# Optimization experiments

Measured on AMD Instinct MI355X. Metric: run time of the kernel, lower is better.

Reference implementation:

```python
import jax, jax.numpy as jnp
import numpy as np

B, L, D, H, DK, DV = 2, 2048, 512, 8, 64, 64
EPS_LN = 1e-6


def setup_inputs() -> dict:
    key = jax.random.key(0)
    ks = jax.random.split(key, 14)
    ws = 0.02  # weight init scale
    inp = {}
    for i, n in enumerate(["q_r", "q_i", "k_r", "k_i", "v_r", "v_i"]):
        inp[n] = jax.random.normal(ks[i], (B, L, D), jnp.float32)
    for j, n in enumerate(["wq_r", "wq_i", "wk_r", "wk_i", "wv_r", "wv_i", "fc_r", "fc_i"]):
        inp[n] = jax.random.normal(ks[6 + j], (D, D), jnp.float32) * ws
    # complextorch CVLayerNorm affine: (2,2,D) weight, diag = 1/sqrt(2); complex bias = 0
    c = np.float32(1.0 / np.sqrt(2.0))
    ln_w = jnp.zeros((2, 2, D), jnp.float32).at[0, 0].set(c).at[1, 1].set(c)
    inp["ln_w"] = ln_w
    inp["ln_b_r"] = jnp.zeros((D,), jnp.float32)
    inp["ln_b_i"] = jnp.zeros((D,), jnp.float32)
    return inp


def _cv_layernorm(x, ln_w, ln_b_r, ln_b_i):
    # covariance-whitening complex LayerNorm over last dim (complextorch style)
    xr, xi = jnp.real(x), jnp.imag(x)
    xr = xr - jnp.mean(xr, axis=-1, keepdims=True)
    xi = xi - jnp.mean(xi, axis=-1, keepdims=True)
    vrr = jnp.mean(xr * xr, axis=-1, keepdims=True) + EPS_LN
    vii = jnp.mean(xi * xi, axis=-1, keepdims=True) + EPS_LN
    vri = jnp.mean(xr * xi, axis=-1, keepdims=True)
    s = jnp.sqrt(vrr * vii - vri * vri)
    t = jnp.sqrt(vrr + vii + 2.0 * s)
    inv = 1.0 / (s * t)
    rrr, rii, rri = (vii + s) * inv, (vrr + s) * inv, -vri * inv
    yr = rrr * xr + rri * xi
    yi = rri * xr + rii * xi
    out_r = ln_w[0, 0] * yr + ln_w[0, 1] * yi + ln_b_r
    out_i = ln_w[1, 0] * yr + ln_w[1, 1] * yi + ln_b_i
    return out_r, out_i


def _mha(q_r, q_i, k_r, k_i, v_r, v_i, wq_r, wq_i, wk_r, wk_i, wv_r, wv_i,
         fc_r, fc_i, ln_w, ln_b_r, ln_b_i):
    q = (q_r + 1j * q_i).astype(jnp.complex64)
    k = (k_r + 1j * k_i).astype(jnp.complex64)
    v = (v_r + 1j * v_i).astype(jnp.complex64)
    Wq = (wq_r + 1j * wq_i).astype(jnp.complex64)
    Wk = (wk_r + 1j * wk_i).astype(jnp.complex64)
    Wv = (wv_r + 1j * wv_i).astype(jnp.complex64)
    Wfc = (fc_r + 1j * fc_i).astype(jnp.complex64)
    b, lq = q.shape[0], q.shape[1]
    # complex linear projections (torch Linear: y = x @ W^T), split into heads
    qh = jnp.einsum('bld,ed->ble', q, Wq).reshape(b, lq, H, DK).transpose(0, 2, 1, 3)
    kh = jnp.einsum('bld,ed->ble', k, Wk).reshape(b, -1, H, DK).transpose(0, 2, 1, 3)
    vh = jnp.einsum('bld,ed->ble', v, Wv).reshape(b, -1, H, DV).transpose(0, 2, 1, 3)
    temp = jnp.float32(DK ** 0.5)
    attn = jnp.einsum('bhqd,bhkd->bhqk', qh / temp, kh)  # [B,H,Lq,Lk] complex
    # CVSoftMax: softmax over magnitude, phase preserved
    mag = jnp.abs(attn)
    w = jax.nn.softmax(mag, axis=-1)
    attn = (w * jnp.exp(1j * jnp.angle(attn))).astype(jnp.complex64)
    out = jnp.einsum('bhqk,bhkd->bhqd', attn, vh)
    out = out.transpose(0, 2, 1, 3).reshape(b, lq, H * DV)
    out = jnp.einsum('ble,de->bld', out, Wfc)
    x = out + q  # residual (dropout is identity at p=0 / eval)
    return _cv_layernorm(x, ln_w, ln_b_r, ln_b_i)


def reference(q_r, q_i, k_r, k_i, v_r, v_i, wq_r, wq_i, wk_r, wk_i, wv_r, wv_i,
              fc_r, fc_i, ln_w, ln_b_r, ln_b_i):
    out_r, out_i = _mha(q_r, q_i, k_r, k_i, v_r, v_i, wq_r, wq_i, wk_r, wk_i,
                        wv_r, wv_i, fc_r, fc_i, ln_w, ln_b_r, ln_b_i)
    # stack real/imag so output is a real float32 tensor [B, L, D, 2]
    return jnp.stack([out_r, out_i], axis=-1)
```

## Files before the change

### kernel.cpp

```cpp
#include <hip/hip_runtime.h>
#include <hip/hip_bf16.h>
#include <math.h>

#define NB 2
#define NL 2048
#define ND 512
#define NH 8
#define NDK 64
#define NROW (NB*NL)
#define HEADSZ (NB*NH*NL*NDK)
#define SEG_BIG ((size_t)NROW*ND)

typedef __attribute__((ext_vector_type(8))) short bf16x8;
typedef __attribute__((ext_vector_type(4))) float f32x4;

__device__ __align__(16) short g_bq_r[HEADSZ], g_bq_i[HEADSZ];
__device__ __align__(16) short g_bk_r[HEADSZ], g_bk_i[HEADSZ];
__device__ __align__(16) short g_bv_r[HEADSZ], g_bv_i[HEADSZ];
__device__ __align__(16) short g_bo_r[SEG_BIG], g_bo_i[SEG_BIG];
__device__ float g_x_r[SEG_BIG];
__device__ float g_x_i[SEG_BIG];

static __device__ __forceinline__ unsigned pack_bf2(float lo, float hi) {
    __hip_bfloat162 h = __float22bfloat162_rn(make_float2(lo, hi));
    unsigned u;
    __builtin_memcpy(&u, &h, 4);
    return u;
}
static __device__ __forceinline__ uint4 ld_cvt(const float* p) {
    const float4 a = *(const float4*)p;
    const float4 b = *(const float4*)(p + 4);
    uint4 o;
    o.x = pack_bf2(a.x, a.y); o.y = pack_bf2(a.z, a.w);
    o.z = pack_bf2(b.x, b.y); o.w = pack_bf2(b.z, b.w);
    return o;
}
static __device__ __forceinline__ bf16x8 negbf(bf16x8 v) {
    #pragma unroll
    for (int e = 0; e < 8; ++e) v[e] ^= (short)0x8000;
    return v;
}

struct GPtrs {
    const float* xr[3]; const float* xi[3];
    const float* wr[4]; const float* wi[4];
    const float* rr; const float* ri;
};

template<int MODE>
__global__ __launch_bounds__(256, 2)
void bgemm(GPtrs gp)
{
    __shared__ __align__(16) short sAr[64][64], sAi[64][64];
    __shared__ __align__(16) short sBr[64][64], sBi[64][64];

    const int bm = blockIdx.x, bn = blockIdx.y;
    const int which = (MODE == 0) ? blockIdx.z : 3;
    const int tx = threadIdx.x;
    const int wave = tx >> 6, lane = tx & 63;
    const int l15 = lane & 15, l4 = lane >> 4;

    const float* Xr = nullptr;
    const float* Xi = nullptr;
    if constexpr (MODE == 0) { Xr = gp.xr[which]; Xi = gp.xi[which]; }
    const float* Wr = gp.wr[which];
    const float* Wi = gp.wi[which];

    const int t0r = tx >> 3;
    const int t0g = tx & 7;

    f32x4 Cr[4] = {}, Ci[4] = {};

    for (int kk = 0; kk < ND; kk += 64) {
        uint4 va0, va1, va2, va3, vb0, vb1, vb2, vb3;
        {
            const size_t a0 = (size_t)(bm*64 + t0r)*ND + kk + t0g*8;
            const size_t a1 = a0 + (size_t)32*ND;
            if constexpr (MODE == 0) {
                va0 = ld_cvt(Xr + a0); va1 = ld_cvt(Xi + a0);
                va2 = ld_cvt(Xr + a1); va3 = ld_cvt(Xi + a1);
            } else {
                va0 = *(const uint4*)(g_bo_r + a0); va1 = *(const uint4*)(g_bo_i + a0);
                va2 = *(const uint4*)(g_bo_r + a1); va3 = *(const uint4*)(g_bo_i + a1);
            }
            const size_t b0 = (size_t)(bn*64 + t0r)*ND + kk + t0g*8;
            const size_t b1 = b0 + (size_t)32*ND;
            vb0 = ld_cvt(Wr + b0); vb1 = ld_cvt(Wi + b0);
            vb2 = ld_cvt(Wr + b1); vb3 = ld_cvt(Wi + b1);
        }
        __syncthreads();
        {
            const int g0 = (t0g ^ (t0r & 7)) << 3;
            const int g1 = (t0g ^ ((t0r + 32) & 7)) << 3;
            *(uint4*)&sAr[t0r][g0]    = va0;
            *(uint4*)&sAi[t0r][g0]    = va1;
            *(uint4*)&sAr[t0r+32][g1] = va2;
            *(uint4*)&sAi[t0r+32][g1] = va3;
            *(uint4*)&sBr[t0r][g0]    = vb0;
            *(uint4*)&sBi[t0r][g0]    = vb1;
            *(uint4*)&sBr[t0r+32][g1] = vb2;
            *(uint4*)&sBi[t0r+32][g1] = vb3;
        }
        __syncthreads();

        #pragma unroll
        for (int ks = 0; ks < 2; ++ks) {
            const int arow = 16*wave + l15;
            const int ag = ((ks*4 + l4) ^ (arow & 7)) << 3;
            const bf16x8 aAr = *(const bf16x8*)&sAr[arow][ag];
            const bf16x8 aAi = *(const bf16x8*)&sAi[arow][ag];
            const bf16x8 aAn = negbf(aAi);
            #pragma unroll
            for (int nt = 0; nt < 4; ++nt) {
                const int brow = nt*16 + l15;
                const int bg = ((ks*4 + l4) ^ (brow & 7)) << 3;
                const bf16x8 bBr = *(const bf16x8*)&sBr[brow][bg];
                const bf16x8 bBi = *(const bf16x8*)&sBi[brow][bg];
                Cr[nt] = __builtin_amdgcn_mfma_f32_16x16x32_bf16(aAr, bBr, Cr[nt], 0, 0, 0);
                Cr[nt] = __builtin_amdgcn_mfma_f32_16x16x32_bf16(aAn, bBi, Cr[nt], 0, 0, 0);
                Ci[nt] = __builtin_amdgcn_mfma_f32_16x16x32_bf16(aAr, bBi, Ci[nt], 0, 0, 0);
                Ci[nt] = __builtin_amdgcn_mfma_f32_16x16x32_bf16(aAi, bBr, Ci[nt], 0, 0, 0);
            }
        }
    }

    const int m0 = bm*64 + 16*wave + 4*l4;
    if constexpr (MODE == 0) {
        if (which == 2) {
            const int bb = m0 >> 11, ll = m0 & (NL-1);
            #pragma unroll
            for (int nt = 0; nt < 4; ++nt) {
                const int d = nt*16 + l15;
                const int lswz = (ll & ~63) | (((((ll >> 3) & 7) ^ (d & 7))) << 3) | (ll & 7);
                const size_t base = ((size_t)(bb*NH + bn)*NDK + d)*NL + lswz;
                *(uint2*)(g_bv_r + base) = make_uint2(pack_bf2(Cr[nt][0], Cr[nt][1]),
                                                      pack_bf2(Cr[nt][2], Cr[nt][3]));
                *(uint2*)(g_bv_i + base) = make_uint2(pack_bf2(Ci[nt][0], Ci[nt][1]),
                                                      pack_bf2(Ci[nt][2], Ci[nt][3]));
            }
        } else {
            const float s = (which == 0) ? 0.125f : 1.0f;
            short* Pr = (which == 0) ? g_bq_r : g_bk_r;
            short* Pi = (which == 0) ? g_bq_i : g_bk_i;
            #pragma unroll
            for (int r = 0; r < 4; ++r) {
                const int m = m0 + r;
                const int bb = m >> 11, ll = m & (NL-1);
                const size_t base = ((size_t)(bb*NH + bn)*NL + ll)*NDK;
                #pragma unroll
                for (int nt = 0; nt < 4; ++nt) {
                    int col = nt*16 + l15;
                    if (which == 1)
                        col = (col & 7) | ((((col >> 3) ^ (ll & 7))) << 3);
                    const unsigned pk = pack_bf2(Cr[nt][r]*s, Ci[nt][r]*s);
                    Pr[base + col] = (short)(pk & 0xFFFFu);
                    Pi[base + col] = (short)(pk >> 16);
                }
            }
        }
    } else {
        const float* Rr = gp.rr;
        const float* Ri = gp.ri;
        #pragma unroll
        for (int r = 0; r < 4; ++r) {
            const int m = m0 + r;
            const size_t base = (size_t)m*ND + bn*64;
            #pragma unroll
            for (int nt = 0; nt < 4; ++nt) {
                const size_t idx = base + nt*16 + l15;
                g_x_r[idx] = Cr[nt][r] + Rr[idx];
                g_x_i[idx] = Ci[nt][r] + Ri[idx];
            }
        }
    }
}

__global__ __launch_bounds__(256, 2)
void cattn()
{
    __shared__ __align__(16) short sKV[2][16384];
    __shared__ __align__(16) short sCr[64][64], sCi[64][64];

    const int nb = blockIdx.x;
    const int xcd = nb & 7, rest = nb >> 3;
    const int bh = xcd*2 + (rest >> 5);
    const int q0 = (rest & 31) * 64;
    const int b = bh >> 3, h = bh & 7;

    const int tx = threadIdx.x;
    const int wave = tx >> 6, lane = tx & 63;
    const int l15 = lane & 15, l4 = lane >> 4;

    const short* Kr = g_bk_r + (size_t)bh*NL*NDK;
    const short* Ki = g_bk_i + (size_t)bh*NL*NDK;
    const short* Vr = g_bv_r + (size_t)bh*NDK*NL;
    const short* Vi = g_bv_i + (size_t)bh*NDK*NL;

    bf16x8 aQr[2], aQi[2], aQn[2];
    {
        const size_t qb = ((size_t)bh*NL + q0 + 16*wave + l15)*NDK + 8*l4;
        aQr[0] = *(const bf16x8*)(g_bq_r + qb);
        aQr[1] = *(const bf16x8*)(g_bq_r + qb + 32);
        aQi[0] = *(const bf16x8*)(g_bq_i + qb);
        aQi[1] = *(const bf16x8*)(g_bq_i + qb + 32);
        aQn[0] = negbf(aQi[0]); aQn[1] = negbf(aQi[1]);
    }

    f32x4 Or[4] = {}, Oi[4] = {};
    float ws[4] = {0.f, 0.f, 0.f, 0.f};

    const short* kvplane = (wave == 0) ? Kr : (wave == 1) ? Ki : (wave == 2) ? Vr : Vi;
    const bool isV = wave >= 2;
    const int pbase = wave * 4096;

    #define STAGE_KV(CHUNK, BUF) do {                                         \
        _Pragma("unroll")                                                     \
        for (int i_ = 0; i_ < 8; ++i_) {                                      \
            const int u_ = i_*64 + lane;                                      \
            const size_t src_ = isV                                           \
                ? (size_t)(u_ >> 3)*NL + (CHUNK)*64 + (u_ & 7)*8              \
                : (size_t)(CHUNK)*4096 + (size_t)u_*8;                        \
            __builtin_amdgcn_global_load_lds(                                 \
                (const __attribute__((address_space(1))) void*)               \
                    (kvplane + src_),                                         \
                (__attribute__((address_space(3))) void*)                     \
                    &sKV[BUF][pbase + u_*8], 16, 0, 0);                       \
        }                                                                     \
    } while (0)

    STAGE_KV(0, 0);
    asm volatile("s_waitcnt vmcnt(0)" ::: "memory");
    __syncthreads();

    const float LOG2E = 1.44269504f;
    const float SHIFT = -4.0f*1.44269504f;

    for (int t = 0; t < 32; ++t) {
        const int cur = t & 1, nxt = cur ^ 1;
        if (t < 31) STAGE_KV(t + 1, nxt);

        #pragma unroll
        for (int tt = 0; tt < 4; ++tt) {
            const int row = tt*16 + l15;
            const int swb = row & 7;
            f32x4 Sr = {}, Si = {};
            __builtin_amdgcn_s_setprio(1);
            #pragma unroll
            for (int c = 0; c < 2; ++c) {
                const int off = (((c*4 + l4) ^ swb) << 3);
                const bf16x8 bKr = *(const bf16x8*)&sKV[cur][row*64 + off];
                const bf16x8 bKi = *(const bf16x8*)&sKV[cur][4096 + row*64 + off];
                Sr = __builtin_amdgcn_mfma_f32_16x16x32_bf16(aQr[c], bKr, Sr, 0, 0, 0);
                Sr = __builtin_amdgcn_mfma_f32_16x16x32_bf16(aQn[c], bKi, Sr, 0, 0, 0);
                Si = __builtin_amdgcn_mfma_f32_16x16x32_bf16(aQr[c], bKi, Si, 0, 0, 0);
                Si = __builtin_amdgcn_mfma_f32_16x16x32_bf16(aQi[c], bKr, Si, 0, 0, 0);
            }
            __builtin_amdgcn_s_setprio(0);
            #pragma unroll
            for (int r = 0; r < 4; ++r) {
                const int qrow = 16*wave + 4*l4 + r;
                const float s2 = fmaxf(fmaf(Sr[r], Sr[r], Si[r]*Si[r]), 1e-30f);
                const float irs = __builtin_amdgcn_rsqf(s2);
                const float mag = s2 * irs;
                const float w = exp2f(fmaf(mag, LOG2E, SHIFT));
                const float sc = w * irs;
                ws[r] += w;
                const int col = (row & 7) | ((((row >> 3) ^ (qrow & 7))) << 3);
                const unsigned pk = pack_bf2(Sr[r]*sc, Si[r]*sc);
                sCr[qrow][col] = (short)(pk & 0xFFFFu);
                sCi[qrow][col] = (short)(pk >> 16);
            }
        }

        asm volatile("s_waitcnt lgkmcnt(0)" ::: "memory");
        __builtin_amdgcn_sched_barrier(0);

        bf16x8 aCr[2], aCi[2], aCn[2];
        {
            const int qrow = 16*wave + l15;
            const int swb = qrow & 7;
            #pragma unroll
            for (int c = 0; c < 2; ++c) {
                const int off = (((c*4 + l4) ^ swb) << 3);
                aCr[c] = *(const bf16x8*)&sCr[qrow][off];
                aCi[c] = *(const bf16x8*)&sCi[qrow][off];
                aCn[c] = negbf(aCi[c]);
            }
        }
        #pragma unroll
        for (int tt = 0; tt < 4; ++tt) {
            const int vrow = tt*16 + l15;
            const int swb = vrow & 7;
            #pragma unroll
            for (int c = 0; c < 2; ++c) {
                const int off = (((c*4 + l4) ^ swb) << 3);
                const bf16x8 bVr = *(const bf16x8*)&sKV[cur][8192  + vrow*64 + off];
                const bf16x8 bVi = *(const bf16x8*)&sKV[cur][12288 + vrow*64 + off];
                Or[tt] = __builtin_amdgcn_mfma_f32_16x16x32_bf16(aCr[c], bVr, Or[tt], 0, 0, 0);
                Or[tt] = __builtin_amdgcn_mfma_f32_16x16x32_bf16(aCn[c], bVi, Or[tt], 0, 0, 0);
                Oi[tt] = __builtin_amdgcn_mfma_f32_16x16x32_bf16(aCr[c], bVi, Oi[tt], 0, 0, 0);
                Oi[tt] = __builtin_amdgcn_mfma_f32_16x16x32_bf16(aCi[c], bVr, Oi[tt], 0, 0, 0);
            }
        }

        asm volatile("s_waitcnt vmcnt(0)" ::: "memory");
        __syncthreads();
    }

    #pragma unroll
    for (int r = 0; r < 4; ++r) {
        #pragma unroll
        for (int off = 8; off; off >>= 1) ws[r] += __shfl_xor(ws[r], off);
    }
    float inv[4];
    #pragma unroll
    for (int r = 0; r < 4; ++r) inv[r] = 1.0f / ws[r];
    #pragma unroll
    for (int t = 0; t < 4; ++t) {
        const int d = t*16 + l15;
        #pragma unroll
        for (int r = 0; r < 4; ++r) {
            const int q = q0 + 16*wave + 4*l4 + r;
            const size_t idx = ((size_t)b*NL + q)*ND + h*NDK + d;
            const unsigned pk = pack_bf2(Or[t][r]*inv[r], Oi[t][r]*inv[r]);
            g_bo_r[idx] = (short)(pk & 0xFFFFu);
            g_bo_i[idx] = (short)(pk >> 16);
        }
    }
    #undef STAGE_KV
}

__global__ __launch_bounds__(256)
void cvln(const float* __restrict__ ln_w, const float* __restrict__ lnb_r,
          const float* __restrict__ lnb_i, float2* __restrict__ out)
{
    __shared__ float red[4][5];
    const int row = blockIdx.x, tx = threadIdx.x;
    const float* xr = g_x_r + (size_t)row*ND;
    const float* xi = g_x_i + (size_t)row*ND;
    const float a0 = xr[tx], a1 = xr[tx+256];
    const float b0 = xi[tx], b1 = xi[tx+256];
    float s_r = a0 + a1, s_i = b0 + b1;
    float srr = a0*a0 + a1*a1, sii = b0*b0 + b1*b1, sri = a0*b0 + a1*b1;
    #pragma unroll
    for (int off = 32; off; off >>= 1) {
        s_r += __shfl_xor(s_r, off);  s_i += __shfl_xor(s_i, off);
        srr += __shfl_xor(srr, off);  sii += __shfl_xor(sii, off);
        sri += __shfl_xor(sri, off);
    }
    const int wave = tx >> 6, lane = tx & 63;
    if (lane == 0) { red[wave][0]=s_r; red[wave][1]=s_i; red[wave][2]=srr; red[wave][3]=sii; red[wave][4]=sri; }
    __syncthreads();
    s_r = red[0][0]+red[1][0]+red[2][0]+red[3][0];
    s_i = red[0][1]+red[1][1]+red[2][1]+red[3][1];
    srr = red[0][2]+red[1][2]+red[2][2]+red[3][2];
    sii = red[0][3]+red[1][3]+red[2][3]+red[3][3];
    sri = red[0][4]+red[1][4]+red[2][4]+red[3][4];

    const float invD = 1.0f/ND;
    const float mr = s_r*invD, mi = s_i*invD;
    const float vrr = srr*invD - mr*mr + 1e-6f;
    const float vii = sii*invD - mi*mi + 1e-6f;
    const float vri = sri*invD - mr*mi;
    const float s  = sqrtf(vrr*vii - vri*vri);
    const float t  = sqrtf(vrr + vii + 2.0f*s);
    const float inv = 1.0f/(s*t);
    const float rrr = (vii + s)*inv, rii = (vrr + s)*inv, rri = -vri*inv;

    #pragma unroll
    for (int p = 0; p < 2; ++p) {
        const int d = tx + p*256;
        const float cxr = (p ? a1 : a0) - mr;
        const float cxi = (p ? b1 : b0) - mi;
        const float yr = rrr*cxr + rri*cxi;
        const float yi = rri*cxr + rii*cxi;
        const float w00 = ln_w[d], w01 = ln_w[512 + d];
        const float w10 = ln_w[1024 + d], w11 = ln_w[1536 + d];
        out[(size_t)row*ND + d] = make_float2(w00*yr + w01*yi + lnb_r[d],
                                              w10*yr + w11*yi + lnb_i[d]);
    }
}

extern "C" void kernel_launch(void* const* d_in, const int* in_sizes, int n_in,
                              void* d_out, int out_size, void* d_ws, size_t ws_size,
                              hipStream_t stream)
{
    (void)in_sizes; (void)n_in; (void)d_ws; (void)ws_size; (void)out_size;
    const float* ln_w = (const float*)d_in[14];
    const float* lnbr = (const float*)d_in[15];
    const float* lnbi = (const float*)d_in[16];

    GPtrs gp;
    gp.xr[0] = (const float*)d_in[0];  gp.xi[0] = (const float*)d_in[1];
    gp.xr[1] = (const float*)d_in[2];  gp.xi[1] = (const float*)d_in[3];
    gp.xr[2] = (const float*)d_in[4];  gp.xi[2] = (const float*)d_in[5];
    gp.wr[0] = (const float*)d_in[6];  gp.wi[0] = (const float*)d_in[7];
    gp.wr[1] = (const float*)d_in[8];  gp.wi[1] = (const float*)d_in[9];
    gp.wr[2] = (const float*)d_in[10]; gp.wi[2] = (const float*)d_in[11];
    gp.wr[3] = (const float*)d_in[12]; gp.wi[3] = (const float*)d_in[13];
    gp.rr = (const float*)d_in[0];     gp.ri = (const float*)d_in[1];

    bgemm<0><<<dim3(NROW/64, ND/64, 3), 256, 0, stream>>>(gp);
    cattn<<<512, 256, 0, stream>>>();
    bgemm<1><<<dim3(NROW/64, ND/64), 256, 0, stream>>>(gp);
    cvln<<<NROW, 256, 0, stream>>>(ln_w, lnbr, lnbi, (float2*)d_out);
}
```

Measured before the change: 177.3 us.

## Split attention key range across two blocks and combine partials in a new kernel

Each attention block now processes half of the keys in 32-key chunks, doubling the grid to 1024 blocks and raising the occupancy target. The V projection is written in a chunk-contiguous swizzled layout so staging is a plain contiguous copy, and the shared-memory footprint is halved. Because softmax uses a fixed shift, the partial numerators and weight sums are written in fp32 to global buffers and merged by a new combine kernel. The trade is extra global traffic for the partial outputs and one more launch.

```diff
diff --git a/kernel.cpp b/kernel.cpp
--- a/kernel.cpp
+++ b/kernel.cpp
@@ -20,6 +20,8 @@
 __device__ __align__(16) short g_bo_r[SEG_BIG], g_bo_i[SEG_BIG];
 __device__ float g_x_r[SEG_BIG];
 __device__ float g_x_i[SEG_BIG];
+__device__ __align__(16) float2 g_po[(size_t)2*16*NL*NDK];
+__device__ float g_pw[(size_t)2*16*NL];
 
 static __device__ __forceinline__ unsigned pack_bf2(float lo, float hi) {
     __hip_bfloat162 h = __float22bfloat162_rn(make_float2(lo, hi));
@@ -128,15 +130,17 @@
     if constexpr (MODE == 0) {
         if (which == 2) {
             const int bb = m0 >> 11, ll = m0 & (NL-1);
+            const int c = ll >> 5, lgrp = (ll >> 3) & 3, e = ll & 7;
             #pragma unroll
             for (int nt = 0; nt < 4; ++nt) {
                 const int d = nt*16 + l15;
-                const int lswz = (ll & ~63) | (((((ll >> 3) & 7) ^ (d & 7))) << 3) | (ll & 7);
-                const size_t base = ((size_t)(bb*NH + bn)*NDK + d)*NL + lswz;
-                *(uint2*)(g_bv_r + base) = make_uint2(pack_bf2(Cr[nt][0], Cr[nt][1]),
-                                                      pack_bf2(Cr[nt][2], Cr[nt][3]));
-                *(uint2*)(g_bv_i + base) = make_uint2(pack_bf2(Ci[nt][0], Ci[nt][1]),
-                                                      pack_bf2(Ci[nt][2], Ci[nt][3]));
+                const int r = d & 31, dpart = d >> 5;
+                const int p = (4*dpart + lgrp) ^ (r & 7);
+                const size_t off = (size_t)(bb*NH + bn)*(NL*NDK) + (size_t)c*2048 + (r*8 + p)*8 + e;
+                *(uint2*)(g_bv_r + off) = make_uint2(pack_bf2(Cr[nt][0], Cr[nt][1]),
+                                                     pack_bf2(Cr[nt][2], Cr[nt][3]));
+                *(uint2*)(g_bv_i + off) = make_uint2(pack_bf2(Ci[nt][0], Ci[nt][1]),
+                                                     pack_bf2(Ci[nt][2], Ci[nt][3]));
             }
         } else {
             const float s = (which == 0) ? 0.125f : 1.0f;
@@ -175,17 +179,18 @@
     }
 }
 
-__global__ __launch_bounds__(256, 2)
+__global__ __launch_bounds__(256, 4)
 void cattn()
 {
-    __shared__ __align__(16) short sKV[2][16384];
-    __shared__ __align__(16) short sCr[64][64], sCi[64][64];
+    __shared__ __align__(16) short sKV[2][8192];
+    __shared__ __align__(16) short sCr[64][32], sCi[64][32];
 
     const int nb = blockIdx.x;
     const int xcd = nb & 7, rest = nb >> 3;
-    const int bh = xcd*2 + (rest >> 5);
-    const int q0 = (rest & 31) * 64;
-    const int b = bh >> 3, h = bh & 7;
+    const int bh = xcd*2 + (rest >> 6);
+    const int within = rest & 63;
+    const int q0 = (within >> 1) * 64;
+    const int half = within & 1;
 
     const int tx = threadIdx.x;
     const int wave = tx >> 6, lane = tx & 63;
@@ -193,8 +198,8 @@
 
     const short* Kr = g_bk_r + (size_t)bh*NL*NDK;
     const short* Ki = g_bk_i + (size_t)bh*NL*NDK;
-    const short* Vr = g_bv_r + (size_t)bh*NDK*NL;
-    const short* Vi = g_bv_i + (size_t)bh*NDK*NL;
+    const short* Vr = g_bv_r + (size_t)bh*NL*NDK;
+    const short* Vi = g_bv_i + (size_t)bh*NL*NDK;
 
     bf16x8 aQr[2], aQi[2], aQn[2];
     {
@@ -210,25 +215,22 @@
     float ws[4] = {0.f, 0.f, 0.f, 0.f};
 
     const short* kvplane = (wave == 0) ? Kr : (wave == 1) ? Ki : (wave == 2) ? Vr : Vi;
-    const bool isV = wave >= 2;
-    const int pbase = wave * 4096;
+    const int pbase = wave * 2048;
 
     #define STAGE_KV(CHUNK, BUF) do {                                         \
         _Pragma("unroll")                                                     \
-        for (int i_ = 0; i_ < 8; ++i_) {                                      \
+        for (int i_ = 0; i_ < 4; ++i_) {                                      \
             const int u_ = i_*64 + lane;                                      \
-            const size_t src_ = isV                                           \
-                ? (size_t)(u_ >> 3)*NL + (CHUNK)*64 + (u_ & 7)*8              \
-                : (size_t)(CHUNK)*4096 + (size_t)u_*8;                        \
             __builtin_amdgcn_global_load_lds(                                 \
                 (const __attribute__((address_space(1))) void*)               \
-                    (kvplane + src_),                                         \
+                    (kvplane + (size_t)(CHUNK)*2048 + (size_t)u_*8),          \
                 (__attribute__((address_space(3))) void*)                     \
                     &sKV[BUF][pbase + u_*8], 16, 0, 0);                       \
         }                                                                     \
     } while (0)
 
-    STAGE_KV(0, 0);
+    const int cbase = half * 32;
+    STAGE_KV(cbase, 0);
     asm volatile("s_waitcnt vmcnt(0)" ::: "memory");
     __syncthreads();
 
@@ -237,10 +239,10 @@
 
     for (int t = 0; t < 32; ++t) {
         const int cur = t & 1, nxt = cur ^ 1;
-        if (t < 31) STAGE_KV(t + 1, nxt);
-
-        #pragma unroll
-        for (int tt = 0; tt < 4; ++tt) {
+        if (t < 31) STAGE_KV(cbase + t + 1, nxt);
+
+        #pragma unroll
+        for (int tt = 0; tt < 2; ++tt) {
             const int row = tt*16 + l15;
             const int swb = row & 7;
             f32x4 Sr = {}, Si = {};
@@ -249,13 +251,14 @@
             for (int c = 0; c < 2; ++c) {
                 const int off = (((c*4 + l4) ^ swb) << 3);
                 const bf16x8 bKr = *(const bf16x8*)&sKV[cur][row*64 + off];
-                const bf16x8 bKi = *(const bf16x8*)&sKV[cur][4096 + row*64 + off];
+                const bf16x8 bKi = *(const bf16x8*)&sKV[cur][2048 + row*64 + off];
                 Sr = __builtin_amdgcn_mfma_f32_16x16x32_bf16(aQr[c], bKr, Sr, 0, 0, 0);
                 Sr = __builtin_amdgcn_mfma_f32_16x16x32_bf16(aQn[c], bKi, Sr, 0, 0, 0);
                 Si = __builtin_amdgcn_mfma_f32_16x16x32_bf16(aQr[c], bKi, Si, 0, 0, 0);
                 Si = __builtin_amdgcn_mfma_f32_16x16x32_bf16(aQi[c], bKr, Si, 0, 0, 0);
             }
             __builtin_amdgcn_s_setprio(0);
+            const int kgrp = row >> 3;
             #pragma unroll
             for (int r = 0; r < 4; ++r) {
                 const int qrow = 16*wave + 4*l4 + r;
@@ -265,7 +268,7 @@
                 const float w = exp2f(fmaf(mag, LOG2E, SHIFT));
                 const float sc = w * irs;
                 ws[r] += w;
-                const int col = (row & 7) | ((((row >> 3) ^ (qrow & 7))) << 3);
+                const int col = (row & 7) | ((kgrp ^ (qrow & 3)) << 3);
                 const unsigned pk = pack_bf2(Sr[r]*sc, Si[r]*sc);
                 sCr[qrow][col] = (short)(pk & 0xFFFFu);
                 sCi[qrow][col] = (short)(pk >> 16);
@@ -275,33 +278,29 @@
         asm volatile("s_waitcnt lgkmcnt(0)" ::: "memory");
         __builtin_amdgcn_sched_barrier(0);
 
-        bf16x8 aCr[2], aCi[2], aCn[2];
+        bf16x8 aCr, aCi, aCn;
         {
             const int qrow = 16*wave + l15;
-            const int swb = qrow & 7;
-            #pragma unroll
-            for (int c = 0; c < 2; ++c) {
-                const int off = (((c*4 + l4) ^ swb) << 3);
-                aCr[c] = *(const bf16x8*)&sCr[qrow][off];
-                aCi[c] = *(const bf16x8*)&sCi[qrow][off];
-                aCn[c] = negbf(aCi[c]);
-            }
-        }
+            const int off = (l4 ^ (qrow & 3)) << 3;
+            aCr = *(const bf16x8*)&sCr[qrow][off];
+            aCi = *(const bf16x8*)&sCi[qrow][off];
+            aCn = negbf(aCi);
+        }
+        __builtin_amdgcn_s_setprio(1);
         #pragma unroll
         for (int tt = 0; tt < 4; ++tt) {
-            const int vrow = tt*16 + l15;
-            const int swb = vrow & 7;
-            #pragma unroll
-            for (int c = 0; c < 2; ++c) {
-                const int off = (((c*4 + l4) ^ swb) << 3);
-                const bf16x8 bVr = *(const bf16x8*)&sKV[cur][8192  + vrow*64 + off];
-                const bf16x8 bVi = *(const bf16x8*)&sKV[cur][12288 + vrow*64 + off];
-                Or[tt] = __builtin_amdgcn_mfma_f32_16x16x32_bf16(aCr[c], bVr, Or[tt], 0, 0, 0);
-                Or[tt] = __builtin_amdgcn_mfma_f32_16x16x32_bf16(aCn[c], bVi, Or[tt], 0, 0, 0);
-                Oi[tt] = __builtin_amdgcn_mfma_f32_16x16x32_bf16(aCr[c], bVi, Oi[tt], 0, 0, 0);
-                Oi[tt] = __builtin_amdgcn_mfma_f32_16x16x32_bf16(aCi[c], bVr, Oi[tt], 0, 0, 0);
-            }
-        }
+            const int d = tt*16 + l15;
+            const int r = d & 31, dpart = tt >> 1;
+            const int p = (4*dpart + l4) ^ (r & 7);
+            const int vb = r*64 + p*8;
+            const bf16x8 bVr = *(const bf16x8*)&sKV[cur][4096 + vb];
+            const bf16x8 bVi = *(const bf16x8*)&sKV[cur][6144 + vb];
+            Or[tt] = __builtin_amdgcn_mfma_f32_16x16x32_bf16(aCr, bVr, Or[tt], 0, 0, 0);
+            Or[tt] = __builtin_amdgcn_mfma_f32_16x16x32_bf16(aCn, bVi, Or[tt], 0, 0, 0);
+            Oi[tt] = __builtin_amdgcn_mfma_f32_16x16x32_bf16(aCr, bVi, Oi[tt], 0, 0, 0);
+            Oi[tt] = __builtin_amdgcn_mfma_f32_16x16x32_bf16(aCi, bVr, Oi[tt], 0, 0, 0);
+        }
+        __builtin_amdgcn_s_setprio(0);
 
         asm volatile("s_waitcnt vmcnt(0)" ::: "memory");
         __syncthreads();
@@ -312,22 +311,41 @@
         #pragma unroll
         for (int off = 8; off; off >>= 1) ws[r] += __shfl_xor(ws[r], off);
     }
-    float inv[4];
+    const size_t pb = (size_t)(half*16 + bh)*NL;
+    if (l15 == 0) {
+        #pragma unroll
+        for (int r = 0; r < 4; ++r)
+            g_pw[pb + q0 + 16*wave + 4*l4 + r] = ws[r];
+    }
     #pragma unroll
-    for (int r = 0; r < 4; ++r) inv[r] = 1.0f / ws[r];
-    #pragma unroll
-    for (int t = 0; t < 4; ++t) {
-        const int d = t*16 + l15;
+    for (int tt = 0; tt < 4; ++tt) {
+        const int d = tt*16 + l15;
         #pragma unroll
         for (int r = 0; r < 4; ++r) {
             const int q = q0 + 16*wave + 4*l4 + r;
-            const size_t idx = ((size_t)b*NL + q)*ND + h*NDK + d;
-            const unsigned pk = pack_bf2(Or[t][r]*inv[r], Oi[t][r]*inv[r]);
-            g_bo_r[idx] = (short)(pk & 0xFFFFu);
-            g_bo_i[idx] = (short)(pk >> 16);
+            g_po[(pb + q)*NDK + d] = make_float2(Or[tt][r], Oi[tt][r]);
         }
     }
     #undef STAGE_KV
+}
+
+__global__ __launch_bounds__(256)
+void comb()
+{
+    const size_t idx = (size_t)blockIdx.x*256 + threadIdx.x;
+    const int d = (int)(idx & 63);
+    const int q = (int)((idx >> 6) & (NL-1));
+    const int bh = (int)(idx >> 17);
+    const size_t p = ((size_t)bh*NL + q)*NDK + d;
+    const float2 a = g_po[p];
+    const float2 c = g_po[(size_t)16*NL*NDK + p];
+    const float w = g_pw[(size_t)bh*NL + q] + g_pw[(size_t)(16 + bh)*NL + q];
+    const float inv = 1.0f / w;
+    const int b = bh >> 3, h = bh & 7;
+    const size_t o = ((size_t)b*NL + q)*ND + h*NDK + d;
+    const unsigned pk = pack_bf2((a.x + c.x)*inv, (a.y + c.y)*inv);
+    g_bo_r[o] = (short)(pk & 0xFFFFu);
+    g_bo_i[o] = (short)(pk >> 16);
 }
 
 __global__ __launch_bounds__(256)
@@ -401,7 +419,8 @@
     gp.rr = (const float*)d_in[0];     gp.ri = (const float*)d_in[1];
 
     bgemm<0><<<dim3(NROW/64, ND/64, 3), 256, 0, stream>>>(gp);
-    cattn<<<512, 256, 0, stream>>>();
+    cattn<<<1024, 256, 0, stream>>>();
+    comb<<<8192, 256, 0, stream>>>();
     bgemm<1><<<dim3(NROW/64, ND/64), 256, 0, stream>>>(gp);
     cvln<<<NROW, 256, 0, stream>>>(ln_w, lnbr, lnbi, (float2*)d_out);
 }
```

Result: no change. 176.6 us (-0.4%).
